# Optimization experiments

Measured on AMD Instinct MI355X. Metric: run time of the kernel, lower is better.

The kernel has to match this reference:

```python
import jax, jax.numpy as jnp
import numpy as np

B, S, D = 16, 4096, 1024
NUM_DISEASES, NUM_STATES = 14, 2
THRESHOLD = 0.2


def setup_inputs() -> dict:
    key = jax.random.key(0)
    k1, k2 = jax.random.split(key)
    z_fused = jax.random.normal(k1, (B, S, D), dtype=jnp.float32)
    # xavier_uniform on M viewed as (num_diseases, num_states, d): fan per torch is
    # fan_in = num_states * d (last two dims flattened receptive field), fan_out = num_diseases... 
    # torch xavier on a 3D tensor: fan_in = D (last dim), fan_out = NUM_STATES, with receptive field = D.
    # Faithful enough init scale: limit = sqrt(6 / (fan_in + fan_out)).
    fan_in = NUM_STATES * D
    fan_out = NUM_DISEASES * D
    limit = float(np.sqrt(6.0 / (fan_in + fan_out)))
    M = jax.random.uniform(k2, (NUM_DISEASES, NUM_STATES, D), dtype=jnp.float32, minval=-limit, maxval=limit)
    return {"z_fused": z_fused, "M": M}


def reference(z_fused, M):
    d = z_fused.shape[-1]
    # mean pool over sequence -> [B, d]
    z_pooled = jnp.mean(z_fused, axis=1)
    # scores: [B, num_diseases, num_states]
    scores = jnp.einsum('bd,nsd->bns', z_pooled, M) / jnp.sqrt(jnp.asarray(d, z_fused.dtype))
    alpha = jax.nn.softmax(scores, axis=-1)
    mlc_probs = alpha[:, :, 1]                      # [B, num_diseases]
    alpha_hat = (mlc_probs > THRESHOLD).astype(z_fused.dtype)
    M_present = M[:, 1, :]                          # [num_diseases, d]
    R = alpha_hat @ M_present                       # [B, d]
    z_out = z_fused + R[:, None, :]                 # broadcast add over S
    return (z_out, mlc_probs)
```

## Files before the change

### kernel.cpp

```cpp
#include <hip/hip_runtime.h>
#include <math.h>

#define BB 16
#define SS 4096
#define DD 1024
#define ND 14
#define THRESH 0.2f

__global__ void pool_partial(const float4* __restrict__ z,
                             float4* __restrict__ part, int rows) {
    const int b = blockIdx.x;
    const int c = blockIdx.y;
    const int t = threadIdx.x;
    const float4* p = z + ((size_t)b * SS + (size_t)c * rows) * (DD / 4) + t;
    float4 acc = {0.f, 0.f, 0.f, 0.f};
#pragma unroll 4
    for (int s = 0; s < rows; ++s) {
        float4 v = p[(size_t)s * (DD / 4)];
        acc.x += v.x; acc.y += v.y; acc.z += v.z; acc.w += v.w;
    }
    part[((size_t)b * gridDim.y + c) * (DD / 4) + t] = acc;
}

__global__ void score_kernel(const float4* __restrict__ part,
                             const float* __restrict__ M,
                             float4* __restrict__ Rout,
                             float* __restrict__ mlc_out, int chunks) {
    const int b = blockIdx.x;
    const int t = threadIdx.x;

    __shared__ float pooled[DD];
    __shared__ float red[4];
    __shared__ float sc[ND * 2];
    __shared__ float hat[ND];

    float4 acc = {0.f, 0.f, 0.f, 0.f};
    const float4* p = part + (size_t)b * chunks * (DD / 4) + t;
    for (int c = 0; c < chunks; ++c) {
        float4 v = p[(size_t)c * (DD / 4)];
        acc.x += v.x; acc.y += v.y; acc.z += v.z; acc.w += v.w;
    }
    const float inv = 1.0f / (float)SS;
    ((float4*)pooled)[t] = make_float4(acc.x * inv, acc.y * inv,
                                       acc.z * inv, acc.w * inv);
    __syncthreads();

    for (int idx = 0; idx < ND * 2; ++idx) {
        const float* Mrow = M + (size_t)idx * DD;
        float partial = 0.f;
        for (int k = t; k < DD; k += 256) partial += pooled[k] * Mrow[k];
        for (int off = 32; off > 0; off >>= 1)
            partial += __shfl_down(partial, off, 64);
        if ((t & 63) == 0) red[t >> 6] = partial;
        __syncthreads();
        if (t == 0) sc[idx] = (red[0] + red[1] + red[2] + red[3]) * (1.0f / 32.0f);
        __syncthreads();
    }

    if (t < ND) {
        float a1 = 1.0f / (1.0f + expf(sc[2 * t] - sc[2 * t + 1]));
        mlc_out[b * ND + t] = a1;
        hat[t] = (a1 > THRESH) ? 1.0f : 0.0f;
    }
    __syncthreads();

    float4 r = {0.f, 0.f, 0.f, 0.f};
    const float4* M4 = (const float4*)M;
    for (int n = 0; n < ND; ++n) {
        if (hat[n] != 0.0f) {
            float4 m = M4[(size_t)(n * 2 + 1) * (DD / 4) + t];
            r.x += m.x; r.y += m.y; r.z += m.z; r.w += m.w;
        }
    }
    Rout[b * (DD / 4) + t] = r;
}

__global__ void add_kernel(const float4* __restrict__ z,
                           const float4* __restrict__ R,
                           float4* __restrict__ out) {
    const int row = blockIdx.x;
    const int t = threadIdx.x;
    const int b = row >> 12;
    const size_t base = (size_t)row * (DD / 4) + t;
    float4 v = z[base];
    float4 r = R[b * (DD / 4) + t];
    v.x += r.x; v.y += r.y; v.z += r.z; v.w += r.w;
    out[base] = v;
}

extern "C" void kernel_launch(void* const* d_in, const int* in_sizes, int n_in,
                              void* d_out, int out_size, void* d_ws, size_t ws_size,
                              hipStream_t stream) {
    const float* z = (const float*)d_in[0];
    const float* M = (const float*)d_in[1];
    float* out = (float*)d_out;

    float* Rws = (float*)d_ws;
    float* part = Rws + (size_t)BB * DD;
    size_t avail = ws_size > (size_t)BB * DD * sizeof(float)
                       ? ws_size - (size_t)BB * DD * sizeof(float) : 0;
    int chunks = 128;
    while (chunks > 1 && (size_t)BB * chunks * DD * sizeof(float) > avail)
        chunks >>= 1;
    const int rows = SS / chunks;

    pool_partial<<<dim3(BB, chunks), 256, 0, stream>>>(
        (const float4*)z, (float4*)part, rows);
    score_kernel<<<BB, 256, 0, stream>>>(
        (const float4*)part, M, (float4*)Rws,
        out + (size_t)BB * SS * DD, chunks);
    add_kernel<<<BB * SS, 256, 0, stream>>>(
        (const float4*)z, (const float4*)Rws, (float4*)out);
}
```

Before: 566.4 us.

## Batch add kernel rows per block with nontemporal loads/stores, parallelize score dot products

The add kernel now processes 32 rows per block over a 16x128 grid, loads R once per block, and uses nontemporal loads and stores to stream the large tensor without polluting cache. The score kernel gives each wave 7 of the 28 dot products, removing the per-score block-wide synchronizations. Pool unroll is raised to 8 and launch bounds are added. Fewer blocks in the add kernel may reduce memory-level parallelism per CU, and nontemporal hints may not help on this hardware.

```diff
diff --git a/kernel.cpp b/kernel.cpp
--- a/kernel.cpp
+++ b/kernel.cpp
@@ -7,14 +7,19 @@
 #define ND 14
 #define THRESH 0.2f
 
-__global__ void pool_partial(const float4* __restrict__ z,
-                             float4* __restrict__ part, int rows) {
+#define ADD_CH 128
+#define AROWS (SS / ADD_CH)
+
+typedef float vfloat4 __attribute__((ext_vector_type(4)));
+
+__global__ __launch_bounds__(256) void pool_partial(
+        const float4* __restrict__ z, float4* __restrict__ part, int rows) {
     const int b = blockIdx.x;
     const int c = blockIdx.y;
     const int t = threadIdx.x;
     const float4* p = z + ((size_t)b * SS + (size_t)c * rows) * (DD / 4) + t;
     float4 acc = {0.f, 0.f, 0.f, 0.f};
-#pragma unroll 4
+#pragma unroll 8
     for (int s = 0; s < rows; ++s) {
         float4 v = p[(size_t)s * (DD / 4)];
         acc.x += v.x; acc.y += v.y; acc.z += v.z; acc.w += v.w;
@@ -22,15 +27,15 @@
     part[((size_t)b * gridDim.y + c) * (DD / 4) + t] = acc;
 }
 
-__global__ void score_kernel(const float4* __restrict__ part,
-                             const float* __restrict__ M,
-                             float4* __restrict__ Rout,
-                             float* __restrict__ mlc_out, int chunks) {
+__global__ __launch_bounds__(256) void score_kernel(
+        const float4* __restrict__ part, const float* __restrict__ M,
+        float4* __restrict__ Rout, float* __restrict__ mlc_out, int chunks) {
     const int b = blockIdx.x;
     const int t = threadIdx.x;
+    const int wave = t >> 6;
+    const int lane = t & 63;
 
     __shared__ float pooled[DD];
-    __shared__ float red[4];
     __shared__ float sc[ND * 2];
     __shared__ float hat[ND];
 
@@ -45,17 +50,17 @@
                                        acc.z * inv, acc.w * inv);
     __syncthreads();
 
-    for (int idx = 0; idx < ND * 2; ++idx) {
+    for (int i = 0; i < 7; ++i) {
+        const int idx = wave * 7 + i;
         const float* Mrow = M + (size_t)idx * DD;
         float partial = 0.f;
-        for (int k = t; k < DD; k += 256) partial += pooled[k] * Mrow[k];
+#pragma unroll
+        for (int k = lane; k < DD; k += 64) partial += pooled[k] * Mrow[k];
         for (int off = 32; off > 0; off >>= 1)
             partial += __shfl_down(partial, off, 64);
-        if ((t & 63) == 0) red[t >> 6] = partial;
-        __syncthreads();
-        if (t == 0) sc[idx] = (red[0] + red[1] + red[2] + red[3]) * (1.0f / 32.0f);
-        __syncthreads();
+        if (lane == 0) sc[idx] = partial * (1.0f / 32.0f);
     }
+    __syncthreads();
 
     if (t < ND) {
         float a1 = 1.0f / (1.0f + expf(sc[2 * t] - sc[2 * t + 1]));
@@ -75,17 +80,21 @@
     Rout[b * (DD / 4) + t] = r;
 }
 
-__global__ void add_kernel(const float4* __restrict__ z,
-                           const float4* __restrict__ R,
-                           float4* __restrict__ out) {
-    const int row = blockIdx.x;
+__global__ __launch_bounds__(256) void add_kernel(
+        const vfloat4* __restrict__ z, const vfloat4* __restrict__ R,
+        vfloat4* __restrict__ out) {
+    const int b = blockIdx.x;
+    const int c = blockIdx.y;
     const int t = threadIdx.x;
-    const int b = row >> 12;
-    const size_t base = (size_t)row * (DD / 4) + t;
-    float4 v = z[base];
-    float4 r = R[b * (DD / 4) + t];
-    v.x += r.x; v.y += r.y; v.z += r.z; v.w += r.w;
-    out[base] = v;
+    const vfloat4 r = R[b * (DD / 4) + t];
+    const size_t base = ((size_t)b * SS + (size_t)c * AROWS) * (DD / 4) + t;
+#pragma unroll 8
+    for (int s = 0; s < AROWS; ++s) {
+        const size_t idx = base + (size_t)s * (DD / 4);
+        vfloat4 v = __builtin_nontemporal_load(&z[idx]);
+        v += r;
+        __builtin_nontemporal_store(v, &out[idx]);
+    }
 }
 
 extern "C" void kernel_launch(void* const* d_in, const int* in_sizes, int n_in,
@@ -102,6 +111,7 @@
     int chunks = 128;
     while (chunks > 1 && (size_t)BB * chunks * DD * sizeof(float) > avail)
         chunks >>= 1;
+    if (chunks < 1) chunks = 1;
     const int rows = SS / chunks;
 
     pool_partial<<<dim3(BB, chunks), 256, 0, stream>>>(
@@ -109,6 +119,6 @@
     score_kernel<<<BB, 256, 0, stream>>>(
         (const float4*)part, M, (float4*)Rws,
         out + (size_t)BB * SS * DD, chunks);
-    add_kernel<<<BB * SS, 256, 0, stream>>>(
-        (const float4*)z, (const float4*)Rws, (float4*)out);
+    add_kernel<<<dim3(BB, ADD_CH), 256, 0, stream>>>(
+        (const vfloat4*)z, (const vfloat4*)Rws, (vfloat4*)out);
 }
```

Result: faster. 551.6 us (-2.6%).
